# Optimization experiments

Measured on AMD Instinct MI355X. Metric: run time of the kernel, lower is better.

Reference implementation:

```python
import jax, jax.numpy as jnp
import numpy as np
import math

DIM = 768
HEADS = 12
HEAD_DIM = DIM // HEADS
SCALE_PARAM_INIT = 1.0 / math.sqrt(DIM)  # Scale(scale=1/sqrt(dim), init=1.0)


def cosine_norm(x, eps=1e-6):
    norm = jnp.maximum(jnp.linalg.norm(x, axis=-1, keepdims=True), eps)
    return x / norm


def setup_inputs() -> dict:
    key = jax.random.key(0)
    ks = jax.random.split(key, 6)
    B, N = 8, 1024
    x = jax.random.normal(ks[0], (B, N, DIM), dtype=jnp.float32)
    # torch nn.Linear weights are [out, in]; y = x @ W^T
    std = 1.0 / math.sqrt(DIM)
    Wq = jax.random.uniform(ks[1], (DIM, DIM), jnp.float32, -std, std)
    Wk = jax.random.uniform(ks[2], (DIM, DIM), jnp.float32, -std, std)
    Wv = jax.random.uniform(ks[3], (DIM, DIM), jnp.float32, -std, std)
    Wo = jax.random.uniform(ks[4], (DIM, DIM), jnp.float32, -std, std)
    # Scale param s: ones * scale, perturbed slightly for generality
    s_qk = SCALE_PARAM_INIT * (1.0 + 0.1 * jax.random.normal(ks[5], (HEADS, HEAD_DIM), jnp.float32))
    return {"x": x, "Wq": Wq, "Wk": Wk, "Wv": Wv, "Wo": Wo, "s_qk": s_qk}


def reference(x, Wq, Wk, Wv, Wo, s_qk):
    B, N, _ = x.shape
    # projections (torch Linear: x @ W^T)
    q = (x @ Wq.T).reshape(B, N, HEADS, HEAD_DIM)
    k = (x @ Wk.T).reshape(B, N, HEADS, HEAD_DIM)
    v = (x @ Wv.T).reshape(B, N, HEADS, HEAD_DIM)
    # effective scale = s * (init / scale)
    s_eff = s_qk * (1.0 / SCALE_PARAM_INIT)  # [H, D]
    q = cosine_norm(q) * s_eff  # broadcast over [B, N, H, D]
    k = cosine_norm(k) * s_eff
    scale = HEAD_DIM ** 0.5  # note: multiplies logits (nGPT-style)
    # [B, H, N, N]
    logits = jnp.einsum('bqhd,bkhd->bhqk', q, k) * scale
    attn = jax.nn.softmax(logits, axis=-1)
    out = jnp.einsum('bhqk,bkhd->bqhd', attn, v).reshape(B, N, HEADS * HEAD_DIM)
    return out @ Wo.T
```

## Files before the change

### kernel.cpp

```cpp
#include <hip/hip_runtime.h>
#include <hip/hip_bf16.h>
#include <math.h>

#define NDIM 768
#define NHEADS 12
#define HD 64
#define SEQ 1024
#define BATCH 8
#define MROWS (BATCH * SEQ)
#define SQRT_DIM 27.712812921102035f
#define LOG2E 1.4426950408889634f

typedef unsigned short u16;
typedef unsigned int u32;
typedef __attribute__((ext_vector_type(8))) short short8;
typedef __attribute__((ext_vector_type(4))) short bf16x4;
typedef __attribute__((ext_vector_type(4))) float f32x4;
typedef __attribute__((ext_vector_type(16))) float f32x16;

#define MFMA16(a, b, c) __builtin_amdgcn_mfma_f32_16x16x32_bf16(a, b, c, 0, 0, 0)
#define MFMA32(a, b, c) __builtin_amdgcn_mfma_f32_32x32x16_bf16(a, b, c, 0, 0, 0)

#if __has_builtin(__builtin_amdgcn_exp2f)
#define EXP2(x) __builtin_amdgcn_exp2f(x)
#else
#define EXP2(x) exp2f(x)
#endif

__device__ inline u16 f2bf(float f) {
    __hip_bfloat16 h = __float2bfloat16(f);
    return *reinterpret_cast<u16*>(&h);
}

__device__ inline u32 rne_pack(float a, float b) {
    u32 ua = __builtin_bit_cast(u32, a), ub = __builtin_bit_cast(u32, b);
    ua = (ua + 0x7fffu + ((ua >> 16) & 1u)) >> 16;
    ub = (ub + 0x7fffu + ((ub >> 16) & 1u)) >> 16;
    return (ub << 16) | ua;
}

__device__ inline void gl2lds16(const void* g, void* l) {
    __builtin_amdgcn_global_load_lds((const __attribute__((address_space(1))) void*)g,
                                     (__attribute__((address_space(3))) void*)l, 16, 0, 0);
}

__device__ inline void bar() {
    asm volatile("" ::: "memory");
    __builtin_amdgcn_s_barrier();
    asm volatile("" ::: "memory");
}
#define LGKM0 asm volatile("s_waitcnt lgkmcnt(0)" ::: "memory")

__global__ __launch_bounds__(256) void castall(const float* __restrict__ x,
                                               const float* __restrict__ Wq,
                                               const float* __restrict__ Wk,
                                               const float* __restrict__ Wv,
                                               const float* __restrict__ Wo,
                                               u16* __restrict__ xb,
                                               u16* __restrict__ Wqkv,
                                               u16* __restrict__ Wob) {
    const int WB = (NDIM * NDIM) / 1024;
    int blk = blockIdx.x;
    const float* s;
    u16* d;
    int base;
    if (blk < 6144) {
        s = x; d = xb; base = blk * 1024;
    } else {
        int wsel = (blk - 6144) / WB, r = (blk - 6144) % WB;
        base = r * 1024;
        if (wsel == 0)      { s = Wq; d = Wqkv; }
        else if (wsel == 1) { s = Wk; d = Wqkv + NDIM * NDIM; }
        else if (wsel == 2) { s = Wv; d = Wqkv + 2 * NDIM * NDIM; }
        else                { s = Wo; d = Wob; }
    }
    int i = base + threadIdx.x * 4;
    float4 v = *(const float4*)(s + i);
    uint2 o = make_uint2(rne_pack(v.x, v.y), rne_pack(v.z, v.w));
    *(uint2*)(d + i) = o;
}

__global__ __launch_bounds__(512, 2) void gemm256_qkv(const u16* __restrict__ A,
                                                      const u16* __restrict__ B,
                                                      u16* __restrict__ Vt,
                                                      const float* __restrict__ s_qk,
                                                      u16* __restrict__ Qdst,
                                                      u16* __restrict__ Kdst) {
    constexpr int K = NDIM;
    constexpr int NT = K / 64;
    __shared__ __align__(16) u16 As[2][2][128 * 64];
    __shared__ __align__(16) u16 Bs[2][2][128 * 64];

    const int t = threadIdx.x;
    const int wave = t >> 6, lane = t & 63;
    const int quad = lane >> 4, l16 = lane & 15;
    const int wm = wave >> 2, wn = wave & 3;
    const int fx = l16 & 7;

    const int wgid = (blockIdx.x & 7) * 36 + (blockIdx.x >> 3);
    const int bm = (wgid / 9) * 256;
    const int bn = (wgid % 9) * 256;

    f32x4 acc[8][4];
#pragma unroll
    for (int i = 0; i < 8; ++i)
#pragma unroll
        for (int j = 0; j < 4; ++j) acc[i][j] = (f32x4){0.f, 0.f, 0.f, 0.f};

    const int srow = lane >> 3;
    const int schk = (lane & 7) ^ srow;
    auto stg = [&](const u16* src, u16* dst) {
#pragma unroll
        for (int it = 0; it < 2; ++it) {
            const int cb = it * 512 + wave * 64;
            const int r = (cb >> 3) + srow;
            gl2lds16(src + (size_t)r * K + schk * 8, (char*)dst + cb * 16);
        }
    };
    const u16* Ag = A + (size_t)bm * K;
    const u16* Bg = B + (size_t)bn * K;

    stg(Ag,                        As[0][0]);
    stg(Ag + (size_t)128 * K,      As[0][1]);
    stg(Bg,                        Bs[0][0]);
    stg(Bg + (size_t)128 * K,      Bs[0][1]);
    stg(Bg + 64,                   Bs[1][0]);
    stg(Bg + (size_t)128 * K + 64, Bs[1][1]);
    asm volatile("s_waitcnt vmcnt(4)" ::: "memory");
    bar();

    short8 a[4][2], b0[2][2], b1[2][2];
    const int rb0 = (wn & 1) * 64;

#pragma unroll 2
    for (int T = 0; T < NT; ++T) {
        const int db = T & 1;
        u16* Asl = As[db][wm];
        u16* Bsl = Bs[db][wn >> 1];
        const u16* An = Ag + (size_t)(T + 1) * 64;
        const u16* Bn = Bg + (size_t)(T + 2) * 64;

#pragma unroll
        for (int mi = 0; mi < 4; ++mi) {
            const int r = mi * 16 + l16;
#pragma unroll
            for (int kk = 0; kk < 2; ++kk)
                a[mi][kk] = *(const short8*)&Asl[(r * 8 + ((kk * 4 + quad) ^ fx)) * 8];
        }
#pragma unroll
        for (int ni = 0; ni < 2; ++ni) {
            const int r = rb0 + ni * 16 + l16;
#pragma unroll
            for (int kk = 0; kk < 2; ++kk)
                b0[ni][kk] = *(const short8*)&Bsl[(r * 8 + ((kk * 4 + quad) ^ fx)) * 8];
        }
        if (T + 1 < NT) stg(An, As[db ^ 1][0]);
        bar();
        LGKM0;
        __builtin_amdgcn_s_setprio(1);
#pragma unroll
        for (int kk = 0; kk < 2; ++kk)
#pragma unroll
            for (int mi = 0; mi < 4; ++mi)
#pragma unroll
                for (int ni = 0; ni < 2; ++ni)
                    acc[mi][ni] = MFMA16(a[mi][kk], b0[ni][kk], acc[mi][ni]);
        __builtin_amdgcn_s_setprio(0);
        bar();

#pragma unroll
        for (int ni = 0; ni < 2; ++ni) {
            const int r = rb0 + (ni + 2) * 16 + l16;
#pragma unroll
            for (int kk = 0; kk < 2; ++kk)
                b1[ni][kk] = *(const short8*)&Bsl[(r * 8 + ((kk * 4 + quad) ^ fx)) * 8];
        }
        if (T + 1 < NT) stg(An + (size_t)128 * K, As[db ^ 1][1]);
        bar();
        LGKM0;
        __builtin_amdgcn_s_setprio(1);
#pragma unroll
        for (int kk = 0; kk < 2; ++kk)
#pragma unroll
            for (int mi = 0; mi < 4; ++mi)
#pragma unroll
                for (int ni = 0; ni < 2; ++ni)
                    acc[mi][ni + 2] = MFMA16(a[mi][kk], b1[ni][kk], acc[mi][ni + 2]);
        __builtin_amdgcn_s_setprio(0);
        bar();

#pragma unroll
        for (int mi = 0; mi < 4; ++mi) {
            const int r = (mi + 4) * 16 + l16;
#pragma unroll
            for (int kk = 0; kk < 2; ++kk)
                a[mi][kk] = *(const short8*)&Asl[(r * 8 + ((kk * 4 + quad) ^ fx)) * 8];
        }
        if (T + 2 < NT) stg(Bn, Bs[db][0]);
        bar();
        LGKM0;
        __builtin_amdgcn_s_setprio(1);
#pragma unroll
        for (int kk = 0; kk < 2; ++kk)
#pragma unroll
            for (int mi = 0; mi < 4; ++mi)
#pragma unroll
                for (int ni = 0; ni < 2; ++ni)
                    acc[mi + 4][ni + 2] = MFMA16(a[mi][kk], b1[ni][kk], acc[mi + 4][ni + 2]);
        __builtin_amdgcn_s_setprio(0);
        bar();

        if (T + 2 < NT) stg(Bn + (size_t)128 * K, Bs[db][1]);
        bar();
        __builtin_amdgcn_s_setprio(1);
#pragma unroll
        for (int kk = 0; kk < 2; ++kk)
#pragma unroll
            for (int mi = 0; mi < 4; ++mi)
#pragma unroll
                for (int ni = 0; ni < 2; ++ni)
                    acc[mi + 4][ni] = MFMA16(a[mi][kk], b0[ni][kk], acc[mi + 4][ni]);
        __builtin_amdgcn_s_setprio(0);
        if (T + 2 < NT) {
            asm volatile("s_waitcnt vmcnt(4)" ::: "memory");
        } else {
            asm volatile("s_waitcnt vmcnt(0)" ::: "memory");
        }
        bar();
    }

    const int cg = (bn + wn * 64) >> 6;
    if (cg >= 2 * NHEADS) {
        const int h = cg - 2 * NHEADS;
#pragma unroll
        for (int mi = 0; mi < 8; ++mi)
#pragma unroll
            for (int ni = 0; ni < 4; ++ni)
#pragma unroll
                for (int r = 0; r < 4; ++r) {
                    const int row = bm + wm * 128 + mi * 16 + quad * 4 + r;
                    const int dd = ni * 16 + l16;
                    const int bb = row >> 10, n = row & 1023;
                    Vt[(((size_t)(bb * NHEADS + h) * HD + dd) << 10) + n] =
                        f2bf(acc[mi][ni][r]);
                }
    } else {
        const bool isq = cg < NHEADS;
        const int h = isq ? cg : cg - NHEADS;
        u16* dst = isq ? Qdst : Kdst;
        const float ex = isq ? 8.f * LOG2E : 1.f;
        float sq[4];
#pragma unroll
        for (int ni = 0; ni < 4; ++ni)
            sq[ni] = s_qk[h * HD + ni * 16 + l16] * SQRT_DIM * ex;
#pragma unroll
        for (int mi = 0; mi < 8; ++mi)
#pragma unroll
            for (int r = 0; r < 4; ++r) {
                float ss = 0.f;
#pragma unroll
                for (int ni = 0; ni < 4; ++ni) ss += acc[mi][ni][r] * acc[mi][ni][r];
                ss += __shfl_xor(ss, 1, 64);
                ss += __shfl_xor(ss, 2, 64);
                ss += __shfl_xor(ss, 4, 64);
                ss += __shfl_xor(ss, 8, 64);
                float inv = 1.f / fmaxf(sqrtf(ss), 1e-6f);
                const int row = bm + wm * 128 + mi * 16 + quad * 4 + r;
                const int bb = row >> 10, tok = row & 1023;
                u16* o = dst + ((size_t)(bb * NHEADS + h) * SEQ + tok) * HD;
#pragma unroll
                for (int ni = 0; ni < 4; ++ni)
                    o[ni * 16 + l16] = f2bf(acc[mi][ni][r] * sq[ni] * inv);
            }
    }
}

template <int EPI>
__global__ __launch_bounds__(256) void gemm_bf16(const u16* __restrict__ A,
                                                 const u16* __restrict__ B,
                                                 void* __restrict__ C, int N,
                                                 const float* __restrict__ s_qk,
                                                 u16* __restrict__ Qdst,
                                                 u16* __restrict__ Kdst,
                                                 int NX) {
    constexpr int K = NDIM;
    constexpr int NKT = K / 32;
    __shared__ __align__(16) u16 As[2][4096];
    __shared__ __align__(16) u16 Bs[2][4096];
    const int t = threadIdx.x;
    const int wave = t >> 6, lane = t & 63;
    const int quad = lane >> 4, l16 = lane & 15;
    const int wx = (wave & 1) * 64, wy = (wave >> 1) * 64;
    const int blk = blockIdx.x;
    const int xcd = blk & 7, local = blk >> 3;
    const int bm = (xcd * 8 + local / NX) * 128;
    const int bn = (local % NX) * 128;

    f32x4 acc[4][4];
#pragma unroll
    for (int i = 0; i < 4; ++i)
#pragma unroll
        for (int j = 0; j < 4; ++j) acc[i][j] = (f32x4){0.f, 0.f, 0.f, 0.f};

    const int srl = lane >> 2;
    const int skc = (lane & 3) ^ ((lane >> 3) & 3);
    auto stage = [&](int k0, int bsel) {
#pragma unroll
        for (int it = 0; it < 2; ++it) {
            const int cb = it * 256 + wave * 64;
            const int row = (cb >> 6) * 16 + srl;
            gl2lds16(A + (size_t)(bm + row) * K + k0 + skc * 8,
                     (char*)As[bsel] + cb * 16);
            gl2lds16(B + (size_t)(bn + row) * K + k0 + skc * 8,
                     (char*)Bs[bsel] + cb * 16);
        }
    };
    const int fxor = (l16 >> 1) & 3;

    stage(0, 0);
#pragma unroll
    for (int kt = 0; kt < NKT; ++kt) {
        __syncthreads();
        if (kt + 1 < NKT) stage((kt + 1) * 32, (kt + 1) & 1);
        const int b = kt & 1;
        short8 af[4], bfr[4];
#pragma unroll
        for (int i = 0; i < 4; ++i)
            af[i] = *(const short8*)&As[b][
                ((((wy >> 4) + i) * 64 + l16 * 4 + (quad ^ fxor)) * 8)];
#pragma unroll
        for (int j = 0; j < 4; ++j)
            bfr[j] = *(const short8*)&Bs[b][
                ((((wx >> 4) + j) * 64 + l16 * 4 + (quad ^ fxor)) * 8)];
#pragma unroll
        for (int i = 0; i < 4; ++i)
#pragma unroll
            for (int j = 0; j < 4; ++j) acc[i][j] = MFMA16(af[i], bfr[j], acc[i][j]);
    }

    if constexpr (EPI == 0) {
#pragma unroll
        for (int i = 0; i < 4; ++i)
#pragma unroll
            for (int j = 0; j < 4; ++j)
#pragma unroll
                for (int r = 0; r < 4; ++r) {
                    const int row = bm + wy + i * 16 + quad * 4 + r;
                    const int col = bn + wx + j * 16 + l16;
                    ((float*)C)[(size_t)row * N + col] = acc[i][j][r];
                }
    }
}

__global__ __launch_bounds__(256) void attn_mfma(const u16* __restrict__ Qh,
                                                 const u16* __restrict__ Kh,
                                                 const u16* __restrict__ Vt,
                                                 u16* __restrict__ AO) {
    __shared__ __align__(16) u16 Ks[512 * 8];
    __shared__ __align__(16) u16 Vs[512 * 8];
    __shared__ __align__(16) u16 Ps[4 * 32 * 64];

    const int t = threadIdx.x;
    const int wave = t >> 6, lane = t & 63;
    const int l31 = lane & 31, half = lane >> 5;
    const int b = blockIdx.z, h = blockIdx.y, q0 = blockIdx.x * 128;
    const int bh = b * NHEADS + h;
    const u16* Kb = Kh + (size_t)bh * SEQ * HD;
    const u16* Vb = Vt + (size_t)bh * HD * SEQ;
    const int qb = q0 + wave * 32;
    const int pbase = wave * 2048 + l31 * 64;
    const int sw = (l31 & 15);

    short8 qf[4];
#pragma unroll
    for (int tt = 0; tt < 4; ++tt)
        qf[tt] = *(const short8*)(Qh + ((size_t)bh * SEQ + qb + l31) * HD +
                                  tt * 16 + half * 8);

    f32x16 o[2];
#pragma unroll
    for (int dt = 0; dt < 2; ++dt)
#pragma unroll
        for (int r = 0; r < 16; ++r) o[dt][r] = 0.f;
    float lp = 0.f;

    const int arl = lane >> 3;
    const int acc8 = (lane & 7) ^ arl;
    const int fx8 = l31 & 7;

    for (int j0 = 0; j0 < SEQ; j0 += 64) {
        __syncthreads();
#pragma unroll
        for (int it = 0; it < 2; ++it) {
            const int cb = it * 256 + wave * 64;
            const int r0 = (cb >> 6) * 8 + arl;
            gl2lds16(Kb + (size_t)(j0 + r0) * HD + acc8 * 8, (char*)Ks + cb * 16);
            gl2lds16(Vb + (size_t)r0 * SEQ + j0 + acc8 * 8, (char*)Vs + cb * 16);
        }
        asm volatile("s_waitcnt vmcnt(0)" ::: "memory");
        __syncthreads();

#pragma unroll
        for (int kt = 0; kt < 2; ++kt) {
            f32x16 sa;
#pragma unroll
            for (int r = 0; r < 16; ++r) sa[r] = 0.f;
#pragma unroll
            for (int tt = 0; tt < 4; ++tt) {
                short8 kf = *(const short8*)&Ks[
                    (((kt * 4 + (l31 >> 3)) * 64) + fx8 * 8 +
                     ((2 * tt + half) ^ fx8)) * 8];
                sa = MFMA32(kf, qf[tt], sa);
            }
#pragma unroll
            for (int rg = 0; rg < 4; ++rg) {
                float p0 = EXP2(sa[rg * 4 + 0]);
                float p1 = EXP2(sa[rg * 4 + 1]);
                float p2 = EXP2(sa[rg * 4 + 2]);
                float p3 = EXP2(sa[rg * 4 + 3]);
                lp += (p0 + p1) + (p2 + p3);
                uint2 pk = make_uint2(rne_pack(p0, p1), rne_pack(p2, p3));
                const int u = kt * 8 + rg * 2 + half;
                *(uint2*)&Ps[pbase + (u ^ sw) * 4] = pk;
            }
        }

#pragma unroll
        for (int k2 = 0; k2 < 4; ++k2) {
            const int u0 = k2 * 4 + half * 2;
            bf16x4 lo = *(const bf16x4*)&Ps[pbase + ((u0 + 0) ^ sw) * 4];
            bf16x4 hi = *(const bf16x4*)&Ps[pbase + ((u0 + 1) ^ sw) * 4];
            short8 pf = __builtin_shufflevector(lo, hi, 0, 1, 2, 3, 4, 5, 6, 7);
#pragma unroll
            for (int dt = 0; dt < 2; ++dt) {
                short8 vf = *(const short8*)&Vs[
                    (((dt * 4 + (l31 >> 3)) * 64) + fx8 * 8 +
                     ((2 * k2 + half) ^ fx8)) * 8];
                o[dt] = MFMA32(vf, pf, o[dt]);
            }
        }
    }

    const float invl = 1.f / (lp + __shfl_xor(lp, 32, 64));
    u16* ob = AO + (size_t)(b * SEQ + qb + l31) * NDIM + h * HD;
#pragma unroll
    for (int dt = 0; dt < 2; ++dt)
#pragma unroll
        for (int rg = 0; rg < 4; ++rg) {
            bf16x4 ok = {(short)f2bf(o[dt][rg * 4 + 0] * invl),
                         (short)f2bf(o[dt][rg * 4 + 1] * invl),
                         (short)f2bf(o[dt][rg * 4 + 2] * invl),
                         (short)f2bf(o[dt][rg * 4 + 3] * invl)};
            *(bf16x4*)(ob + dt * 32 + rg * 8 + half * 4) = ok;
        }
}

extern "C" void kernel_launch(void* const* d_in, const int* in_sizes, int n_in,
                              void* d_out, int out_size, void* d_ws, size_t ws_size,
                              hipStream_t stream) {
    const float* x    = (const float*)d_in[0];
    const float* Wq   = (const float*)d_in[1];
    const float* Wk   = (const float*)d_in[2];
    const float* Wv   = (const float*)d_in[3];
    const float* Wo   = (const float*)d_in[4];
    const float* s_qk = (const float*)d_in[5];
    float* out = (float*)d_out;

    char* w = (char*)d_ws;
    const size_t TE = (size_t)MROWS * NDIM;
    u16* xb   = (u16*)w;                    w += TE * 2;
    u16* Wqkv = (u16*)w;                    w += (size_t)3 * NDIM * NDIM * 2;
    u16* Wob  = (u16*)w;                    w += (size_t)NDIM * NDIM * 2;
    u16* Qh   = (u16*)w;                    w += TE * 2;
    u16* Kh   = (u16*)w;                    w += TE * 2;
    u16* Vt   = (u16*)w;                    w += TE * 2;
    u16* ao   = (u16*)w;

    castall<<<6144 + 4 * 576, 256, 0, stream>>>(x, Wq, Wk, Wv, Wo, xb, Wqkv, Wob);

    gemm256_qkv<<<288, 512, 0, stream>>>(xb, Wqkv, Vt, s_qk, Qh, Kh);

    attn_mfma<<<dim3(SEQ / 128, NHEADS, BATCH), 256, 0, stream>>>(Qh, Kh, Vt, ao);

    gemm_bf16<0><<<6 * 64, 256, 0, stream>>>(
        ao, Wob, out, NDIM, nullptr, nullptr, nullptr, 6);
}
```

Baseline: 203.3 us.

## Split QKV GEMM into 256x256 tiles plus 128x128 tail tiles for last V heads

Blocks 0-255 now cover output columns 0-2047 with 256x256 tiles mapped so that each XCD owns a contiguous 1024-row band. Extra blocks 256-383 compute the remaining 256 columns (V heads 8-11) with smaller 128x128 tiles on a simple double-buffered loop. The aim is to fill the GPU better and improve L2 locality than the old 288 uniform tiles did. V-transposed stores are also packed into 4-element vector writes instead of scalar stores. The tail blocks use a plain load-wait-compute loop with full vmcnt waits, which may make them less efficient per flop.

```diff
diff --git a/kernel.cpp b/kernel.cpp
--- a/kernel.cpp
+++ b/kernel.cpp
@@ -50,6 +50,7 @@
     asm volatile("" ::: "memory");
 }
 #define LGKM0 asm volatile("s_waitcnt lgkmcnt(0)" ::: "memory")
+#define VM0   asm volatile("s_waitcnt vmcnt(0)" ::: "memory")
 
 __global__ __launch_bounds__(256) void castall(const float* __restrict__ x,
                                                const float* __restrict__ Wq,
@@ -94,18 +95,8 @@
     const int t = threadIdx.x;
     const int wave = t >> 6, lane = t & 63;
     const int quad = lane >> 4, l16 = lane & 15;
-    const int wm = wave >> 2, wn = wave & 3;
     const int fx = l16 & 7;
-
-    const int wgid = (blockIdx.x & 7) * 36 + (blockIdx.x >> 3);
-    const int bm = (wgid / 9) * 256;
-    const int bn = (wgid % 9) * 256;
-
-    f32x4 acc[8][4];
-#pragma unroll
-    for (int i = 0; i < 8; ++i)
-#pragma unroll
-        for (int j = 0; j < 4; ++j) acc[i][j] = (f32x4){0.f, 0.f, 0.f, 0.f};
+    const int blk = blockIdx.x;
 
     const int srow = lane >> 3;
     const int schk = (lane & 7) ^ srow;
@@ -117,161 +108,242 @@
             gl2lds16(src + (size_t)r * K + schk * 8, (char*)dst + cb * 16);
         }
     };
-    const u16* Ag = A + (size_t)bm * K;
-    const u16* Bg = B + (size_t)bn * K;
-
-    stg(Ag,                        As[0][0]);
-    stg(Ag + (size_t)128 * K,      As[0][1]);
-    stg(Bg,                        Bs[0][0]);
-    stg(Bg + (size_t)128 * K,      Bs[0][1]);
-    stg(Bg + 64,                   Bs[1][0]);
-    stg(Bg + (size_t)128 * K + 64, Bs[1][1]);
-    asm volatile("s_waitcnt vmcnt(4)" ::: "memory");
-    bar();
-
-    short8 a[4][2], b0[2][2], b1[2][2];
-    const int rb0 = (wn & 1) * 64;
+
+    if (blk < 256) {
+        const int wm = wave >> 2, wn = wave & 3;
+        const int xcd = blk & 7, local = blk >> 3;
+        const int bm = xcd * 1024 + (local >> 3) * 256;
+        const int bn = (local & 7) * 256;
+
+        f32x4 acc[8][4];
+#pragma unroll
+        for (int i = 0; i < 8; ++i)
+#pragma unroll
+            for (int j = 0; j < 4; ++j) acc[i][j] = (f32x4){0.f, 0.f, 0.f, 0.f};
+
+        const u16* Ag = A + (size_t)bm * K;
+        const u16* Bg = B + (size_t)bn * K;
+
+        stg(Ag,                        As[0][0]);
+        stg(Ag + (size_t)128 * K,      As[0][1]);
+        stg(Bg,                        Bs[0][0]);
+        stg(Bg + (size_t)128 * K,      Bs[0][1]);
+        stg(Bg + 64,                   Bs[1][0]);
+        stg(Bg + (size_t)128 * K + 64, Bs[1][1]);
+        asm volatile("s_waitcnt vmcnt(4)" ::: "memory");
+        bar();
+
+        short8 a[4][2], b0[2][2], b1[2][2];
+        const int rb0 = (wn & 1) * 64;
 
 #pragma unroll 2
-    for (int T = 0; T < NT; ++T) {
-        const int db = T & 1;
-        u16* Asl = As[db][wm];
-        u16* Bsl = Bs[db][wn >> 1];
-        const u16* An = Ag + (size_t)(T + 1) * 64;
-        const u16* Bn = Bg + (size_t)(T + 2) * 64;
-
-#pragma unroll
-        for (int mi = 0; mi < 4; ++mi) {
-            const int r = mi * 16 + l16;
+        for (int T = 0; T < NT; ++T) {
+            const int db = T & 1;
+            u16* Asl = As[db][wm];
+            u16* Bsl = Bs[db][wn >> 1];
+            const u16* An = Ag + (size_t)(T + 1) * 64;
+            const u16* Bn = Bg + (size_t)(T + 2) * 64;
+
+#pragma unroll
+            for (int mi = 0; mi < 4; ++mi) {
+                const int r = mi * 16 + l16;
+#pragma unroll
+                for (int kk = 0; kk < 2; ++kk)
+                    a[mi][kk] = *(const short8*)&Asl[(r * 8 + ((kk * 4 + quad) ^ fx)) * 8];
+            }
+#pragma unroll
+            for (int ni = 0; ni < 2; ++ni) {
+                const int r = rb0 + ni * 16 + l16;
+#pragma unroll
+                for (int kk = 0; kk < 2; ++kk)
+                    b0[ni][kk] = *(const short8*)&Bsl[(r * 8 + ((kk * 4 + quad) ^ fx)) * 8];
+            }
+            if (T + 1 < NT) stg(An, As[db ^ 1][0]);
+            bar();
+            LGKM0;
+            __builtin_amdgcn_s_setprio(1);
 #pragma unroll
             for (int kk = 0; kk < 2; ++kk)
-                a[mi][kk] = *(const short8*)&Asl[(r * 8 + ((kk * 4 + quad) ^ fx)) * 8];
-        }
-#pragma unroll
-        for (int ni = 0; ni < 2; ++ni) {
-            const int r = rb0 + ni * 16 + l16;
+#pragma unroll
+                for (int mi = 0; mi < 4; ++mi)
+#pragma unroll
+                    for (int ni = 0; ni < 2; ++ni)
+                        acc[mi][ni] = MFMA16(a[mi][kk], b0[ni][kk], acc[mi][ni]);
+            __builtin_amdgcn_s_setprio(0);
+            bar();
+
+#pragma unroll
+            for (int ni = 0; ni < 2; ++ni) {
+                const int r = rb0 + (ni + 2) * 16 + l16;
+#pragma unroll
+                for (int kk = 0; kk < 2; ++kk)
+                    b1[ni][kk] = *(const short8*)&Bsl[(r * 8 + ((kk * 4 + quad) ^ fx)) * 8];
+            }
+            if (T + 1 < NT) stg(An + (size_t)128 * K, As[db ^ 1][1]);
+            bar();
+            LGKM0;
+            __builtin_amdgcn_s_setprio(1);
 #pragma unroll
             for (int kk = 0; kk < 2; ++kk)
-                b0[ni][kk] = *(const short8*)&Bsl[(r * 8 + ((kk * 4 + quad) ^ fx)) * 8];
-        }
-        if (T + 1 < NT) stg(An, As[db ^ 1][0]);
+#pragma unroll
+                for (int mi = 0; mi < 4; ++mi)
+#pragma unroll
+                    for (int ni = 0; ni < 2; ++ni)
+                        acc[mi][ni + 2] = MFMA16(a[mi][kk], b1[ni][kk], acc[mi][ni + 2]);
+            __builtin_amdgcn_s_setprio(0);
+            bar();
+
+#pragma unroll
+            for (int mi = 0; mi < 4; ++mi) {
+                const int r = (mi + 4) * 16 + l16;
+#pragma unroll
+                for (int kk = 0; kk < 2; ++kk)
+                    a[mi][kk] = *(const short8*)&Asl[(r * 8 + ((kk * 4 + quad) ^ fx)) * 8];
+            }
+            if (T + 2 < NT) stg(Bn, Bs[db][0]);
+            bar();
+            LGKM0;
+            __builtin_amdgcn_s_setprio(1);
+#pragma unroll
+            for (int kk = 0; kk < 2; ++kk)
+#pragma unroll
+                for (int mi = 0; mi < 4; ++mi)
+#pragma unroll
+                    for (int ni = 0; ni < 2; ++ni)
+                        acc[mi + 4][ni + 2] = MFMA16(a[mi][kk], b1[ni][kk], acc[mi + 4][ni + 2]);
+            __builtin_amdgcn_s_setprio(0);
+            bar();
+
+            if (T + 2 < NT) stg(Bn + (size_t)128 * K, Bs[db][1]);
+            bar();
+            __builtin_amdgcn_s_setprio(1);
+#pragma unroll
+            for (int kk = 0; kk < 2; ++kk)
+#pragma unroll
+                for (int mi = 0; mi < 4; ++mi)
+#pragma unroll
+                    for (int ni = 0; ni < 2; ++ni)
+                        acc[mi + 4][ni] = MFMA16(a[mi][kk], b0[ni][kk], acc[mi + 4][ni]);
+            __builtin_amdgcn_s_setprio(0);
+            if (T + 2 < NT) {
+                asm volatile("s_waitcnt vmcnt(4)" ::: "memory");
+            } else {
+                VM0;
+            }
+            bar();
+        }
+
+        const int cg = (bn + wn * 64) >> 6;
+        if (cg >= 2 * NHEADS) {
+            const int h = cg - 2 * NHEADS;
+#pragma unroll
+            for (int mi = 0; mi < 8; ++mi) {
+                const int row = bm + wm * 128 + mi * 16 + quad * 4;
+                const int bb = row >> 10, n0 = row & 1023;
+#pragma unroll
+                for (int ni = 0; ni < 4; ++ni) {
+                    const int dd = ni * 16 + l16;
+                    uint2 pk = make_uint2(rne_pack(acc[mi][ni][0], acc[mi][ni][1]),
+                                          rne_pack(acc[mi][ni][2], acc[mi][ni][3]));
+                    *(uint2*)(Vt + (((size_t)(bb * NHEADS + h) * HD + dd) << 10) + n0) = pk;
+                }
+            }
+        } else {
+            const bool isq = cg < NHEADS;
+            const int h = isq ? cg : cg - NHEADS;
+            u16* dst = isq ? Qdst : Kdst;
+            const float ex = isq ? 8.f * LOG2E : 1.f;
+            float sq[4];
+#pragma unroll
+            for (int ni = 0; ni < 4; ++ni)
+                sq[ni] = s_qk[h * HD + ni * 16 + l16] * SQRT_DIM * ex;
+#pragma unroll
+            for (int mi = 0; mi < 8; ++mi)
+#pragma unroll
+                for (int r = 0; r < 4; ++r) {
+                    float ss = 0.f;
+#pragma unroll
+                    for (int ni = 0; ni < 4; ++ni) ss += acc[mi][ni][r] * acc[mi][ni][r];
+                    ss += __shfl_xor(ss, 1, 64);
+                    ss += __shfl_xor(ss, 2, 64);
+                    ss += __shfl_xor(ss, 4, 64);
+                    ss += __shfl_xor(ss, 8, 64);
+                    float inv = 1.f / fmaxf(sqrtf(ss), 1e-6f);
+                    const int row = bm + wm * 128 + mi * 16 + quad * 4 + r;
+                    const int bb = row >> 10, tok = row & 1023;
+                    u16* o = dst + ((size_t)(bb * NHEADS + h) * SEQ + tok) * HD;
+#pragma unroll
+                    for (int ni = 0; ni < 4; ++ni)
+                        o[ni * 16 + l16] = f2bf(acc[mi][ni][r] * sq[ni] * inv);
+                }
+        }
+    } else {
+        const int q = blk - 256;
+        const int bm = (q >> 1) * 128;
+        const int bn = 2048 + (q & 1) * 128;
+        const int wm4 = wave >> 1, wn2 = wave & 1;
+        const u16* Aq = A + (size_t)bm * K;
+        const u16* Bq = B + (size_t)bn * K;
+
+        f32x4 qa[2][4];
+#pragma unroll
+        for (int i = 0; i < 2; ++i)
+#pragma unroll
+            for (int j = 0; j < 4; ++j) qa[i][j] = (f32x4){0.f, 0.f, 0.f, 0.f};
+
+        stg(Aq, As[0][0]);
+        stg(Bq, Bs[0][0]);
+        VM0;
         bar();
-        LGKM0;
-        __builtin_amdgcn_s_setprio(1);
-#pragma unroll
-        for (int kk = 0; kk < 2; ++kk)
-#pragma unroll
-            for (int mi = 0; mi < 4; ++mi)
-#pragma unroll
-                for (int ni = 0; ni < 2; ++ni)
-                    acc[mi][ni] = MFMA16(a[mi][kk], b0[ni][kk], acc[mi][ni]);
-        __builtin_amdgcn_s_setprio(0);
-        bar();
-
-#pragma unroll
-        for (int ni = 0; ni < 2; ++ni) {
-            const int r = rb0 + (ni + 2) * 16 + l16;
+#pragma unroll 2
+        for (int T = 0; T < NT; ++T) {
+            const int db = T & 1;
+            if (T + 1 < NT) {
+                stg(Aq + (size_t)(T + 1) * 64, As[db ^ 1][0]);
+                stg(Bq + (size_t)(T + 1) * 64, Bs[db ^ 1][0]);
+            }
+            const u16* Asl = As[db][0];
+            const u16* Bsl = Bs[db][0];
+            short8 af[2][2], bf[4][2];
+#pragma unroll
+            for (int mi = 0; mi < 2; ++mi) {
+                const int r = wm4 * 32 + mi * 16 + l16;
+#pragma unroll
+                for (int kk = 0; kk < 2; ++kk)
+                    af[mi][kk] = *(const short8*)&Asl[(r * 8 + ((kk * 4 + quad) ^ fx)) * 8];
+            }
+#pragma unroll
+            for (int ni = 0; ni < 4; ++ni) {
+                const int r = wn2 * 64 + ni * 16 + l16;
+#pragma unroll
+                for (int kk = 0; kk < 2; ++kk)
+                    bf[ni][kk] = *(const short8*)&Bsl[(r * 8 + ((kk * 4 + quad) ^ fx)) * 8];
+            }
+            __builtin_amdgcn_s_setprio(1);
 #pragma unroll
             for (int kk = 0; kk < 2; ++kk)
-                b1[ni][kk] = *(const short8*)&Bsl[(r * 8 + ((kk * 4 + quad) ^ fx)) * 8];
-        }
-        if (T + 1 < NT) stg(An + (size_t)128 * K, As[db ^ 1][1]);
-        bar();
-        LGKM0;
-        __builtin_amdgcn_s_setprio(1);
-#pragma unroll
-        for (int kk = 0; kk < 2; ++kk)
-#pragma unroll
-            for (int mi = 0; mi < 4; ++mi)
-#pragma unroll
-                for (int ni = 0; ni < 2; ++ni)
-                    acc[mi][ni + 2] = MFMA16(a[mi][kk], b1[ni][kk], acc[mi][ni + 2]);
-        __builtin_amdgcn_s_setprio(0);
-        bar();
-
-#pragma unroll
-        for (int mi = 0; mi < 4; ++mi) {
-            const int r = (mi + 4) * 16 + l16;
-#pragma unroll
-            for (int kk = 0; kk < 2; ++kk)
-                a[mi][kk] = *(const short8*)&Asl[(r * 8 + ((kk * 4 + quad) ^ fx)) * 8];
-        }
-        if (T + 2 < NT) stg(Bn, Bs[db][0]);
-        bar();
-        LGKM0;
-        __builtin_amdgcn_s_setprio(1);
-#pragma unroll
-        for (int kk = 0; kk < 2; ++kk)
-#pragma unroll
-            for (int mi = 0; mi < 4; ++mi)
-#pragma unroll
-                for (int ni = 0; ni < 2; ++ni)
-                    acc[mi + 4][ni + 2] = MFMA16(a[mi][kk], b1[ni][kk], acc[mi + 4][ni + 2]);
-        __builtin_amdgcn_s_setprio(0);
-        bar();
-
-        if (T + 2 < NT) stg(Bn + (size_t)128 * K, Bs[db][1]);
-        bar();
-        __builtin_amdgcn_s_setprio(1);
-#pragma unroll
-        for (int kk = 0; kk < 2; ++kk)
-#pragma unroll
-            for (int mi = 0; mi < 4; ++mi)
-#pragma unroll
-                for (int ni = 0; ni < 2; ++ni)
-                    acc[mi + 4][ni] = MFMA16(a[mi][kk], b0[ni][kk], acc[mi + 4][ni]);
-        __builtin_amdgcn_s_setprio(0);
-        if (T + 2 < NT) {
-            asm volatile("s_waitcnt vmcnt(4)" ::: "memory");
-        } else {
-            asm volatile("s_waitcnt vmcnt(0)" ::: "memory");
-        }
-        bar();
-    }
-
-    const int cg = (bn + wn * 64) >> 6;
-    if (cg >= 2 * NHEADS) {
-        const int h = cg - 2 * NHEADS;
-#pragma unroll
-        for (int mi = 0; mi < 8; ++mi)
-#pragma unroll
-            for (int ni = 0; ni < 4; ++ni)
-#pragma unroll
-                for (int r = 0; r < 4; ++r) {
-                    const int row = bm + wm * 128 + mi * 16 + quad * 4 + r;
-                    const int dd = ni * 16 + l16;
-                    const int bb = row >> 10, n = row & 1023;
-                    Vt[(((size_t)(bb * NHEADS + h) * HD + dd) << 10) + n] =
-                        f2bf(acc[mi][ni][r]);
-                }
-    } else {
-        const bool isq = cg < NHEADS;
-        const int h = isq ? cg : cg - NHEADS;
-        u16* dst = isq ? Qdst : Kdst;
-        const float ex = isq ? 8.f * LOG2E : 1.f;
-        float sq[4];
-#pragma unroll
-        for (int ni = 0; ni < 4; ++ni)
-            sq[ni] = s_qk[h * HD + ni * 16 + l16] * SQRT_DIM * ex;
-#pragma unroll
-        for (int mi = 0; mi < 8; ++mi)
-#pragma unroll
-            for (int r = 0; r < 4; ++r) {
-                float ss = 0.f;
-#pragma unroll
-                for (int ni = 0; ni < 4; ++ni) ss += acc[mi][ni][r] * acc[mi][ni][r];
-                ss += __shfl_xor(ss, 1, 64);
-                ss += __shfl_xor(ss, 2, 64);
-                ss += __shfl_xor(ss, 4, 64);
-                ss += __shfl_xor(ss, 8, 64);
-                float inv = 1.f / fmaxf(sqrtf(ss), 1e-6f);
-                const int row = bm + wm * 128 + mi * 16 + quad * 4 + r;
-                const int bb = row >> 10, tok = row & 1023;
-                u16* o = dst + ((size_t)(bb * NHEADS + h) * SEQ + tok) * HD;
-#pragma unroll
-                for (int ni = 0; ni < 4; ++ni)
-                    o[ni * 16 + l16] = f2bf(acc[mi][ni][r] * sq[ni] * inv);
-            }
+#pragma unroll
+                for (int mi = 0; mi < 2; ++mi)
+#pragma unroll
+                    for (int ni = 0; ni < 4; ++ni)
+                        qa[mi][ni] = MFMA16(af[mi][kk], bf[ni][kk], qa[mi][ni]);
+            __builtin_amdgcn_s_setprio(0);
+            VM0;
+            bar();
+        }
+        const int h = 8 + (q & 1) * 2 + wn2;
+#pragma unroll
+        for (int mi = 0; mi < 2; ++mi) {
+            const int row = bm + wm4 * 32 + mi * 16 + quad * 4;
+            const int bb = row >> 10, n0 = row & 1023;
+#pragma unroll
+            for (int ni = 0; ni < 4; ++ni) {
+                const int dd = ni * 16 + l16;
+                uint2 pk = make_uint2(rne_pack(qa[mi][ni][0], qa[mi][ni][1]),
+                                      rne_pack(qa[mi][ni][2], qa[mi][ni][3]));
+                *(uint2*)(Vt + (((size_t)(bb * NHEADS + h) * HD + dd) << 10) + n0) = pk;
+            }
+        }
     }
 }
 
@@ -478,7 +550,7 @@
 
     castall<<<6144 + 4 * 576, 256, 0, stream>>>(x, Wq, Wk, Wv, Wo, xb, Wqkv, Wob);
 
-    gemm256_qkv<<<288, 512, 0, stream>>>(xb, Wqkv, Vt, s_qk, Qh, Kh);
+    gemm256_qkv<<<384, 512, 0, stream>>>(xb, Wqkv, Vt, s_qk, Qh, Kh);
 
     attn_mfma<<<dim3(SEQ / 128, NHEADS, BATCH), 256, 0, stream>>>(Qh, Kh, Vt, ao);
 
```

Result: faster. 192.4 us (-5.4%).
